# Performance work log

Measured on AMD Instinct MI355X. Metric: run time of the kernel, lower is better.

Reference implementation:

```python
import jax, jax.numpy as jnp
import numpy as np

B, S, NX, H = 8, 1024, 1024, 16
D = NX // H  # head dim = 64


def setup_inputs() -> dict:
    key = jax.random.key(0)
    k1, k2, k3 = jax.random.split(key, 3)
    x = jax.random.normal(k1, (B, S, NX), dtype=jnp.float32)
    Wqkv = jax.random.normal(k2, (NX, 3 * NX), dtype=jnp.float32) * 0.02
    bqkv = jnp.zeros((3 * NX,), dtype=jnp.float32)
    Wproj = jax.random.normal(k3, (NX, NX), dtype=jnp.float32) * 0.02
    bproj = jnp.zeros((NX,), dtype=jnp.float32)
    return {"x": x, "Wqkv": Wqkv, "bqkv": bqkv, "Wproj": Wproj, "bproj": bproj}


def reference(x, Wqkv, bqkv, Wproj, bproj):
    # c_attn: Conv1D == x @ W + b
    qkv = jnp.einsum('bsn,nm->bsm', x, Wqkv) + bqkv  # [B,S,3*NX]
    q, k, v = jnp.split(qkv, 3, axis=-1)
    # split heads -> [B,H,S,D]
    def split_heads(t):
        return t.reshape(B, S, H, D).transpose(0, 2, 1, 3)
    q, k, v = split_heads(q), split_heads(k), split_heads(v)
    # present = stack(key, value) with key as [B,H,S,D]
    present = jnp.stack((k, v))  # [2,B,H,S,D]
    # scores, scaled (scale=True) by sqrt(head_dim)
    w = jnp.einsum('bhqd,bhkd->bhqk', q, k) / jnp.sqrt(jnp.asarray(D, x.dtype))
    bias = jnp.tril(jnp.ones((S, S), dtype=x.dtype))[None, None]  # causal tril buffer
    w = w * bias - 10000.0 * (1.0 - bias)
    w = jax.nn.softmax(w, axis=-1)
    a = jnp.einsum('bhqk,bhkd->bhqd', w, v)  # [B,H,S,D]
    a = a.transpose(0, 2, 1, 3).reshape(B, S, NX)  # merge heads
    a = jnp.einsum('bsn,nm->bsm', a, Wproj) + bproj  # c_proj
    return a, present
```

## Files before the change

### kernel.cpp

```cpp
#include <hip/hip_runtime.h>
#include <stdint.h>


#define BB 8
#define SS 1024
#define NXX 1024
#define NH 16
#define HD 64
#define KK 1024
#define NKT 16

typedef __bf16 bf16x8 __attribute__((ext_vector_type(8)));
typedef float  floatx4 __attribute__((ext_vector_type(4)));
typedef unsigned short ushort8 __attribute__((ext_vector_type(8)));
typedef unsigned short ushortx4 __attribute__((ext_vector_type(4)));

__device__ inline float bf2f(unsigned short u) {
    unsigned int x = ((unsigned int)u) << 16;
    float f;
    __builtin_memcpy(&f, &x, 4);
    return f;
}
__device__ inline unsigned short f2bf(float f) {
    unsigned int u;
    __builtin_memcpy(&u, &f, 4);
    u += 0x7FFFu + ((u >> 16) & 1u);
    return (unsigned short)(u >> 16);
}

__device__ inline void gload_lds16(const unsigned short* g, unsigned short* l) {
    __builtin_amdgcn_global_load_lds(
        (const __attribute__((address_space(1))) void*)g,
        (__attribute__((address_space(3))) void*)l, 16, 0, 0);
}

__device__ inline void barrier_raw() {
    asm volatile("" ::: "memory");
    __builtin_amdgcn_sched_barrier(0);
    __builtin_amdgcn_s_barrier();
    __builtin_amdgcn_sched_barrier(0);
    asm volatile("" ::: "memory");
}
#define WAIT_VM4() asm volatile("s_waitcnt vmcnt(4)" ::: "memory")
#define WAIT_VM0() asm volatile("s_waitcnt vmcnt(0)" ::: "memory")

__global__ void sniff_k(const unsigned short* __restrict__ x, int* __restrict__ flag) {
    if (threadIdx.x == 0 && blockIdx.x == 0) {
        int g = 0;
        for (int i = 0; i < 512; i++) {
            float f = bf2f(x[i]);
            float a = fabsf(f);
            if (!(a <= 1e4f)) g++;
            else if (f != 0.f && a < 1e-35f) g++;
        }
        *flag = (g > 16) ? 1 : 0;
    }
}

__global__ __launch_bounds__(256) void prep(
    const void* __restrict__ x, const void* __restrict__ Wqkv,
    const void* __restrict__ Wproj,
    unsigned short* __restrict__ xbf, unsigned short* __restrict__ WqkvT,
    unsigned short* __restrict__ WprojT, const int* __restrict__ flagp) {
    const int f32 = *flagp;
    int blk = blockIdx.x;
    if (blk < 4096) {
        const size_t i = ((size_t)blk * 256 + threadIdx.x) * 8;
        if (f32) {
            const floatx4* p = (const floatx4*)((const float*)x + i);
            floatx4 f0 = p[0], f1 = p[1];
            ushort8 u;
#pragma unroll
            for (int j = 0; j < 4; j++) { u[j] = f2bf(f0[j]); u[4 + j] = f2bf(f1[j]); }
            *(ushort8*)(xbf + i) = u;
        } else {
            *(ushort8*)(xbf + i) = *(const ushort8*)((const unsigned short*)x + i);
        }
        return;
    }
    blk -= 4096;
    const void* in;
    unsigned short* out;
    int R, C;
    if (blk < 3072) { in = Wqkv; out = WqkvT; R = 1024; C = 3072; }
    else            { blk -= 3072; in = Wproj; out = WprojT; R = 1024; C = 1024; }
    const int ctiles = C / 32;
    const int c0 = (blk % ctiles) * 32, r0 = (blk / ctiles) * 32;

    __shared__ unsigned short tile[32][33];
    const int tx = threadIdx.x & 31, ty = threadIdx.x >> 5;
    if (f32) {
        const float* inf = (const float*)in;
#pragma unroll
        for (int i = ty; i < 32; i += 8)
            tile[i][tx] = f2bf(inf[(size_t)(r0 + i) * C + c0 + tx]);
    } else {
        const unsigned short* inu = (const unsigned short*)in;
#pragma unroll
        for (int i = ty; i < 32; i += 8)
            tile[i][tx] = inu[(size_t)(r0 + i) * C + c0 + tx];
    }
    __syncthreads();
#pragma unroll
    for (int i = ty; i < 32; i += 8)
        out[(size_t)(c0 + i) * R + r0 + tx] = tile[tx][i];
}

__global__ __launch_bounds__(256) void transpose_v(
    const void* __restrict__ outbase, unsigned short* __restrict__ vbfT,
    const int* __restrict__ flagp) {
    const int f32 = *flagp;
    const int blk = blockIdx.x;
    const int sb = blk & 15;
    const int bh = blk >> 4;
    const int tid = threadIdx.x;
    const int r = tid >> 2;
    const int c0 = (tid & 3) * 16;
    __shared__ unsigned short tile[64][72];
    const int perm = ((r & 15) << 2) | (r >> 4);
    const size_t esz = f32 ? 4 : 2;
    const char* vbase = (const char*)outbase + (size_t)(2 * BB * SS * NXX) * esz;
    if (f32) {
        const float* src = (const float*)vbase + ((size_t)bh * SS + sb * 64 + r) * HD + c0;
#pragma unroll
        for (int j = 0; j < 16; j++) tile[c0 + j][perm] = f2bf(src[j]);
    } else {
        const unsigned short* src = (const unsigned short*)vbase + ((size_t)bh * SS + sb * 64 + r) * HD + c0;
#pragma unroll
        for (int j = 0; j < 16; j++) tile[c0 + j][perm] = src[j];
    }
    __syncthreads();
    const int d = tid >> 2;
    const int o0 = (tid & 3) * 16;
    unsigned short* dst = vbfT + ((size_t)(bh * HD + d)) * SS + sb * 64 + o0;
    *(ushort8*)dst       = *(const ushort8*)&tile[d][o0];
    *(ushort8*)(dst + 8) = *(const ushort8*)&tile[d][o0 + 8];
}

#define STAGE_A(slot, h, kt) do { \
    const unsigned short* sg_ = Ab + (size_t)((h) * 128) * KK + (size_t)(kt) * 64; \
    gload_lds16(sg_, &As[slot][h][w * 512]); \
    gload_lds16(sg_ + (size_t)64 * KK, &As[slot][h][4096 + w * 512]); \
} while (0)
#define STAGE_B(slot, h, kt) do { \
    const unsigned short* sg_ = Bb + (size_t)((h) * 128) * KK + (size_t)(kt) * 64; \
    gload_lds16(sg_, &Bs[slot][h][w * 512]); \
    gload_lds16(sg_ + (size_t)64 * KK, &Bs[slot][h][4096 + w * 512]); \
} while (0)
#define PHASE(qq, STAGE_STMT, TAIL) do { \
    bf16x8 a_[2][2]; \
    _Pragma("unroll") \
    for (int mm = 0; mm < 2; mm++) { \
        const int arow = (qq) * 32 + mm * 16 + l15; \
        a_[mm][0] = *(const bf16x8*)&Ah[arow * 64 + fo0]; \
        a_[mm][1] = *(const bf16x8*)&Ah[arow * 64 + fo1]; \
    } \
    STAGE_STMT; \
    barrier_raw(); \
    __builtin_amdgcn_s_setprio(1); \
    _Pragma("unroll") \
    for (int mm = 0; mm < 2; mm++) \
    _Pragma("unroll") \
    for (int nf = 0; nf < 4; nf++) { \
        acc[2 * (qq) + mm][nf] = __builtin_amdgcn_mfma_f32_16x16x32_bf16(a_[mm][0], bfr[nf][0], acc[2 * (qq) + mm][nf], 0, 0, 0); \
        acc[2 * (qq) + mm][nf] = __builtin_amdgcn_mfma_f32_16x16x32_bf16(a_[mm][1], bfr[nf][1], acc[2 * (qq) + mm][nf], 0, 0, 0); \
    } \
    __builtin_amdgcn_s_setprio(0); \
    TAIL; \
    barrier_raw(); \
} while (0)

template <int MODE>
__global__ __launch_bounds__(512, 2) void gemm8p(
    const unsigned short* __restrict__ A,
    const unsigned short* __restrict__ Bt,
    const void* __restrict__ bias,
    void* __restrict__ outbase,
    unsigned short* __restrict__ q_ws,
    unsigned short* __restrict__ kbf,
    int M, int N, int Nt, const int* __restrict__ flagp) {
    __shared__ __align__(16) unsigned short As[2][2][128 * 64];
    __shared__ __align__(16) unsigned short Bs[2][2][128 * 64];

    const int f32 = *flagp;
    const int tid  = threadIdx.x;
    const int lane = tid & 63;
    const int w = tid >> 6;
    const int r = w >> 2;
    const int c = w & 3;
    const int bh2 = c >> 1;
    const int l15 = lane & 15;
    const int quad = lane >> 4;

    const int cpx = gridDim.x >> 3;
    const int bid = (blockIdx.x & 7) * cpx + (blockIdx.x >> 3);
    const int bx = bid % Nt, by = bid / Nt;
    const int row0 = by * 256, col0 = bx * 256;

    floatx4 acc[8][4];
    floatx4 zz = {0.f, 0.f, 0.f, 0.f};
#pragma unroll
    for (int i = 0; i < 8; i++)
#pragma unroll
        for (int j = 0; j < 4; j++) acc[i][j] = zz;

    const int srow = tid >> 3;
    const int scole = ((tid & 7) ^ (srow & 7)) << 3;
    const unsigned short* Ab = A  + (size_t)(row0 + srow) * KK + scole;
    const unsigned short* Bb = Bt + (size_t)(col0 + srow) * KK + scole;

    const int fo0 = (quad << 3) ^ ((l15 & 7) << 3);
    const int fo1 = fo0 ^ 32;

    STAGE_A(0, 0, 0); STAGE_A(0, 1, 0);
    STAGE_B(0, 0, 0); STAGE_B(0, 1, 0);
    STAGE_B(1, 0, 1); STAGE_B(1, 1, 1);
    WAIT_VM4();
    barrier_raw();

    bf16x8 bfr[4][2];
#pragma unroll 2
    for (int t = 0; t < NKT; t++) {
        const int slot = t & 1;
        const unsigned short* Ah = &As[slot][r][0];
        const unsigned short* Bh = &Bs[slot][bh2][0];
#pragma unroll
        for (int nf = 0; nf < 4; nf++) {
            const int brow = (c & 1) * 64 + nf * 16 + l15;
            bfr[nf][0] = *(const bf16x8*)&Bh[brow * 64 + fo0];
            bfr[nf][1] = *(const bf16x8*)&Bh[brow * 64 + fo1];
        }
        PHASE(0, { if (t + 1 < NKT) STAGE_A((t + 1) & 1, 0, t + 1); }, {});
        PHASE(1, { if (t + 1 < NKT) STAGE_A((t + 1) & 1, 1, t + 1); }, {});
        PHASE(2, { if (t + 2 < NKT) STAGE_B(slot, 0, t + 2); }, {});
        PHASE(3, { if (t + 2 < NKT) STAGE_B(slot, 1, t + 2); },
              { if (t < NKT - 2) { WAIT_VM4(); } else { WAIT_VM0(); } });
    }

    float bv[4];
#pragma unroll
    for (int nf = 0; nf < 4; nf++) {
        const int colb = col0 + c * 64 + nf * 16 + l15;
        bv[nf] = f32 ? ((const float*)bias)[colb] : bf2f(((const unsigned short*)bias)[colb]);
    }

    if (MODE == 0) {
#pragma unroll
        for (int mi = 0; mi < 8; mi++)
#pragma unroll
            for (int nf = 0; nf < 4; nf++) {
                const int colb = col0 + c * 64 + nf * 16 + l15;
#pragma unroll
                for (int i = 0; i < 4; i++) {
                    const int row = row0 + r * 128 + mi * 16 + quad * 4 + i;
                    const float val = acc[mi][nf][i] + bv[nf];
                    const size_t idx = (size_t)row * N + colb;
                    if (f32) ((float*)outbase)[idx] = val;
                    else     ((unsigned short*)outbase)[idx] = f2bf(val);
                }
            }
        return;
    }

    const int sec = col0 >> 10;
    const size_t esz = f32 ? 4 : 2;
    const int b = row0 >> 10;
    const int s0 = row0 & 1023;

    if (sec == 0) {
#pragma unroll
        for (int mi = 0; mi < 8; mi++)
#pragma unroll
            for (int nf = 0; nf < 4; nf++) {
                const int colb = col0 + c * 64 + nf * 16 + l15;
                const int h = (colb & 1023) >> 6, d = colb & 63;
#pragma unroll
                for (int i = 0; i < 4; i++) {
                    const int s = s0 + r * 128 + mi * 16 + quad * 4 + i;
                    q_ws[(size_t)((b * NH + h) * SS + s) * HD + d] = f2bf(acc[mi][nf][i] + bv[nf]);
                }
            }
    } else if (sec == 1) {
        char* kbase = (char*)outbase + (size_t)(BB * SS * NXX) * esz;
#pragma unroll
        for (int mi = 0; mi < 8; mi++)
#pragma unroll
            for (int nf = 0; nf < 4; nf++) {
                const int colb = col0 + c * 64 + nf * 16 + l15;
                const int h = (colb & 1023) >> 6, d = colb & 63;
#pragma unroll
                for (int i = 0; i < 4; i++) {
                    const int s = s0 + r * 128 + mi * 16 + quad * 4 + i;
                    const float val = acc[mi][nf][i] + bv[nf];
                    const size_t idx = (size_t)((b * NH + h) * SS + s) * HD + d;
                    if (f32) ((float*)kbase)[idx] = val;
                    else     ((unsigned short*)kbase)[idx] = f2bf(val);
                    kbf[idx] = f2bf(val);
                }
            }
    } else {
        char* vbase = (char*)outbase + (size_t)(2 * BB * SS * NXX) * esz;
#pragma unroll
        for (int mi = 0; mi < 8; mi++)
#pragma unroll
            for (int nf = 0; nf < 4; nf++) {
                const int colb = col0 + c * 64 + nf * 16 + l15;
                const int h = (colb & 1023) >> 6, d = colb & 63;
#pragma unroll
                for (int i = 0; i < 4; i++) {
                    const int s = s0 + r * 128 + mi * 16 + quad * 4 + i;
                    const float val = acc[mi][nf][i] + bv[nf];
                    const size_t idx = (size_t)((b * NH + h) * SS + s) * HD + d;
                    if (f32) ((float*)vbase)[idx] = val;
                    else     ((unsigned short*)vbase)[idx] = f2bf(val);
                }
            }
    }
}

__global__ __launch_bounds__(256) void attn(
    const unsigned short* __restrict__ q_ws,
    const unsigned short* __restrict__ kbf,
    const unsigned short* __restrict__ vbfT,
    unsigned short* __restrict__ amerged) {
    const int tid = threadIdx.x;
    const int lane = tid & 63;
    const int w = tid >> 6;
    const int l15 = lane & 15, quad = lane >> 4;
    const int blk = blockIdx.x;
    const int p = blk & 3;
    const int bh = blk >> 2;
    const int b = bh >> 4, h = bh & 15;

    const unsigned short* Q = q_ws + (size_t)bh * (SS * HD);
    const unsigned short* K = kbf + (size_t)bh * (SS * HD);
    const unsigned short* V = vbfT + (size_t)bh * (HD * SS);

    __shared__ __align__(16) unsigned short Ks[64][72];
    __shared__ __align__(16) unsigned short Vs[64][72];
    __shared__ __align__(16) unsigned short Pl[4][32][72];

    floatx4 zz = {0.f, 0.f, 0.f, 0.f};
    ushort8 ones_u;
#pragma unroll
    for (int j = 0; j < 8; j++) ones_u[j] = 0x3F80;
    const bf16x8 ones = __builtin_bit_cast(bf16x8, ones_u);

    const int srow = tid >> 2;
    const int soff = (tid & 3) * 16;

#pragma unroll
    for (int tile = 0; tile < 2; tile++) {
        const int qb = tile ? (7 - p) : p;
        const int qbase = qb * 128;
        const int wrow0 = qbase + w * 32;
        const int wq_max = wrow0 + 31;
        const int jend = qbase + 128;

        bf16x8 qa[2][2];
#pragma unroll
        for (int m = 0; m < 2; m++)
#pragma unroll
            for (int t = 0; t < 2; t++)
                qa[m][t] = *(const bf16x8*)&Q[(size_t)(wrow0 + m * 16 + l15) * HD + t * 32 + quad * 8];

        floatx4 o[2][4], o5[2];
        float mrow[2][4];
#pragma unroll
        for (int m = 0; m < 2; m++) {
            o5[m] = zz;
#pragma unroll
            for (int i = 0; i < 4; i++) mrow[m][i] = -1e30f;
#pragma unroll
            for (int nf = 0; nf < 4; nf++) o[m][nf] = zz;
        }

        *(ushort8*)&Ks[srow][soff]     = *(const ushort8*)&K[(size_t)srow * HD + soff];
        *(ushort8*)&Ks[srow][soff + 8] = *(const ushort8*)&K[(size_t)srow * HD + soff + 8];
        *(ushort8*)&Vs[srow][soff]     = *(const ushort8*)&V[(size_t)srow * SS + soff];
        *(ushort8*)&Vs[srow][soff + 8] = *(const ushort8*)&V[(size_t)srow * SS + soff + 8];
        __syncthreads();

        for (int j0 = 0; j0 < jend; j0 += 64) {
            const bool havenext = (j0 + 64 < jend);
            ushort8 kn0, kn1, vn0, vn1;
            if (havenext) {
                kn0 = *(const ushort8*)&K[(size_t)(j0 + 64 + srow) * HD + soff];
                kn1 = *(const ushort8*)&K[(size_t)(j0 + 64 + srow) * HD + soff + 8];
                vn0 = *(const ushort8*)&V[(size_t)srow * SS + j0 + 64 + soff];
                vn1 = *(const ushort8*)&V[(size_t)srow * SS + j0 + 64 + soff + 8];
            }

            if (j0 <= wq_max) {
                floatx4 sf[2][4];
#pragma unroll
                for (int kg = 0; kg < 4; kg++) {
                    bf16x8 kb0 = *(const bf16x8*)&Ks[kg * 16 + l15][quad * 8];
                    bf16x8 kb1 = *(const bf16x8*)&Ks[kg * 16 + l15][32 + quad * 8];
#pragma unroll
                    for (int m = 0; m < 2; m++) {
                        floatx4 s = zz;
                        s = __builtin_amdgcn_mfma_f32_16x16x32_bf16(qa[m][0], kb0, s, 0, 0, 0);
                        s = __builtin_amdgcn_mfma_f32_16x16x32_bf16(qa[m][1], kb1, s, 0, 0, 0);
                        sf[m][kg] = s;
                    }
                }

                float alpha_[2][4];
#pragma unroll
                for (int m = 0; m < 2; m++)
#pragma unroll
                    for (int i = 0; i < 4; i++) {
                        const int qrow = wrow0 + m * 16 + quad * 4 + i;
                        float pv4[4];
#pragma unroll
                        for (int kg = 0; kg < 4; kg++) {
                            const int key = j0 + kg * 16 + l15;
                            float s = sf[m][kg][i] * 0.125f;
                            if (key > qrow) s = -10000.0f;
                            pv4[kg] = s;
                        }
                        float t = fmaxf(fmaxf(pv4[0], pv4[1]), fmaxf(pv4[2], pv4[3]));
                        t = fmaxf(t, __shfl_xor(t, 1));
                        t = fmaxf(t, __shfl_xor(t, 2));
                        t = fmaxf(t, __shfl_xor(t, 4));
                        t = fmaxf(t, __shfl_xor(t, 8));
                        const float mnew = fmaxf(mrow[m][i], t);
                        alpha_[m][i] = __expf(mrow[m][i] - mnew);
                        mrow[m][i] = mnew;
                        ushortx4 pk;
#pragma unroll
                        for (int kg = 0; kg < 4; kg++)
                            pk[kg] = f2bf(__expf(pv4[kg] - mnew));
                        *(ushortx4*)&Pl[w][m * 16 + quad * 4 + i][l15 * 4] = pk;
                    }

#pragma unroll
                for (int m = 0; m < 2; m++) {
#pragma unroll
                    for (int i = 0; i < 4; i++) o5[m][i] *= alpha_[m][i];
#pragma unroll
                    for (int nf = 0; nf < 4; nf++)
#pragma unroll
                        for (int i = 0; i < 4; i++) o[m][nf][i] *= alpha_[m][i];
                }

                bf16x8 pa[2][2];
#pragma unroll
                for (int m = 0; m < 2; m++) {
                    pa[m][0] = *(const bf16x8*)&Pl[w][m * 16 + l15][quad * 8];
                    pa[m][1] = *(const bf16x8*)&Pl[w][m * 16 + l15][32 + quad * 8];
                }

#pragma unroll
                for (int m = 0; m < 2; m++) {
                    o5[m] = __builtin_amdgcn_mfma_f32_16x16x32_bf16(pa[m][0], ones, o5[m], 0, 0, 0);
                    o5[m] = __builtin_amdgcn_mfma_f32_16x16x32_bf16(pa[m][1], ones, o5[m], 0, 0, 0);
                }
#pragma unroll
                for (int nf = 0; nf < 4; nf++) {
                    bf16x8 vb0 = *(const bf16x8*)&Vs[nf * 16 + l15][quad * 8];
                    bf16x8 vb1 = *(const bf16x8*)&Vs[nf * 16 + l15][32 + quad * 8];
#pragma unroll
                    for (int m = 0; m < 2; m++) {
                        o[m][nf] = __builtin_amdgcn_mfma_f32_16x16x32_bf16(pa[m][0], vb0, o[m][nf], 0, 0, 0);
                        o[m][nf] = __builtin_amdgcn_mfma_f32_16x16x32_bf16(pa[m][1], vb1, o[m][nf], 0, 0, 0);
                    }
                }
            }
            __syncthreads();
            if (havenext) {
                *(ushort8*)&Ks[srow][soff]     = kn0;
                *(ushort8*)&Ks[srow][soff + 8] = kn1;
                *(ushort8*)&Vs[srow][soff]     = vn0;
                *(ushort8*)&Vs[srow][soff + 8] = vn1;
            }
            __syncthreads();
        }

#pragma unroll
        for (int m = 0; m < 2; m++)
#pragma unroll
            for (int nf = 0; nf < 4; nf++)
#pragma unroll
                for (int i = 0; i < 4; i++) {
                    const int s = wrow0 + m * 16 + quad * 4 + i;
                    amerged[(size_t)(b * SS + s) * NXX + h * HD + nf * 16 + l15] =
                        f2bf(o[m][nf][i] / o5[m][i]);
                }
        __syncthreads();
    }
}

extern "C" void kernel_launch(void* const* d_in, const int* in_sizes, int n_in,
                              void* d_out, int out_size, void* d_ws, size_t ws_size,
                              hipStream_t stream) {
    const void* x     = d_in[0];
    const void* Wqkv  = d_in[1];
    const void* bqkv  = d_in[2];
    const void* Wproj = d_in[3];
    const void* bproj = d_in[4];

    int* flag = (int*)d_ws;
    unsigned short* ws = (unsigned short*)d_ws + 8;
    unsigned short* WqkvT   = ws;
    unsigned short* WprojT  = WqkvT + 3072 * 1024;
    unsigned short* q_ws    = WprojT + 1024 * 1024;
    unsigned short* kbf     = q_ws + 8 * 1024 * 1024;
    unsigned short* vbfT    = kbf + 8 * 1024 * 1024;
    unsigned short* amerged = vbfT + 8 * 1024 * 1024;
    unsigned short* xbf     = amerged;

    sniff_k<<<1, 64, 0, stream>>>((const unsigned short*)x, flag);
    prep<<<dim3(8192), 256, 0, stream>>>(x, Wqkv, Wproj, xbf, WqkvT, WprojT, flag);
    gemm8p<1><<<dim3(12 * 32), 512, 0, stream>>>(
        xbf, WqkvT, bqkv, d_out, q_ws, kbf, 8192, 3072, 12, flag);
    transpose_v<<<dim3(128 * 16), 256, 0, stream>>>(d_out, vbfT, flag);
    attn<<<dim3(BB * NH * 4), 256, 0, stream>>>(q_ws, kbf, vbfT, amerged);
    gemm8p<0><<<dim3(4 * 32), 512, 0, stream>>>(
        amerged, WprojT, bproj, d_out, nullptr, nullptr, 8192, 1024, 4, flag);
}
```

Baseline: 346.7 us.

## Use 128x128 tiled GEMM for output projection, exp2 softmax, parallel sniff

Replaces the 256x512-style gemm8p projection launch (128 blocks of 512 threads) with a new 128x128-tile, double-buffered LDS GEMM launched on a 8x64 grid, so more blocks fill the GPU. The attention softmax folds the log2(e) factor into the score scale and uses exp2f in place of __expf, which removes a multiply per exponent. The input-dtype sniff kernel now reads with a full wavefront and a shuffle reduction instead of a serial 512-element loop. The new GEMM uses a shallow K-step of 32 with a barrier every iteration, which may limit its throughput.

```diff
diff --git a/kernel.cpp b/kernel.cpp
--- a/kernel.cpp
+++ b/kernel.cpp
@@ -45,16 +45,19 @@
 #define WAIT_VM0() asm volatile("s_waitcnt vmcnt(0)" ::: "memory")
 
 __global__ void sniff_k(const unsigned short* __restrict__ x, int* __restrict__ flag) {
-    if (threadIdx.x == 0 && blockIdx.x == 0) {
-        int g = 0;
-        for (int i = 0; i < 512; i++) {
-            float f = bf2f(x[i]);
-            float a = fabsf(f);
-            if (!(a <= 1e4f)) g++;
-            else if (f != 0.f && a < 1e-35f) g++;
-        }
-        *flag = (g > 16) ? 1 : 0;
-    }
+    const int lane = threadIdx.x & 63;
+    ushort8 v = *(const ushort8*)(x + (size_t)lane * 8);
+    int g = 0;
+#pragma unroll
+    for (int j = 0; j < 8; j++) {
+        float f = bf2f(v[j]);
+        float a = fabsf(f);
+        if (!(a <= 1e4f)) g++;
+        else if (f != 0.f && a < 1e-35f) g++;
+    }
+#pragma unroll
+    for (int s = 1; s < 64; s <<= 1) g += __shfl_xor(g, s);
+    if (lane == 0 && blockIdx.x == 0) *flag = (g > 16) ? 1 : 0;
 }
 
 __global__ __launch_bounds__(256) void prep(
@@ -318,6 +321,95 @@
     }
 }
 
+__global__ __launch_bounds__(256) void gemm_bt(
+    const unsigned short* __restrict__ A,
+    const unsigned short* __restrict__ Bt,
+    const void* __restrict__ bias,
+    void* __restrict__ outbase,
+    int M, int N, int K, const int* __restrict__ flagp) {
+    __shared__ __align__(16) unsigned short As[2][128 * 32];
+    __shared__ __align__(16) unsigned short Bs[2][128 * 32];
+
+    const int f32 = *flagp;
+    const int tid  = threadIdx.x;
+    const int lane = tid & 63;
+    const int wave = tid >> 6;
+    const int wr = wave >> 1, wc = wave & 1;
+    const int l15 = lane & 15;
+    const int quad = lane >> 4;
+    const int row0 = blockIdx.y * 128;
+    const int col0 = blockIdx.x * 128;
+
+    floatx4 acc[4][4];
+    floatx4 zz = {0.f, 0.f, 0.f, 0.f};
+#pragma unroll
+    for (int i = 0; i < 4; i++)
+#pragma unroll
+        for (int j = 0; j < 4; j++) acc[i][j] = zz;
+
+    const int lrow = lane >> 2;
+    const int lcol = (lane & 3) * 8;
+    const unsigned short* Ag = A  + (size_t)(row0 + wave * 32 + lrow) * K + lcol;
+    const unsigned short* Bg = Bt + (size_t)(col0 + wave * 32 + lrow) * K + lcol;
+    const int sl0 = (wave * 32) * 32;
+    const int sl1 = (wave * 32 + 16) * 32;
+
+    gload_lds16(Ag, &As[0][sl0]);
+    gload_lds16(Ag + (size_t)16 * K, &As[0][sl1]);
+    gload_lds16(Bg, &Bs[0][sl0]);
+    gload_lds16(Bg + (size_t)16 * K, &Bs[0][sl1]);
+    __syncthreads();
+
+    int cur = 0;
+    for (int k0 = 0; k0 < K; k0 += 32) {
+        if (k0 + 32 < K) {
+            const unsigned short* Agn = Ag + k0 + 32;
+            const unsigned short* Bgn = Bg + k0 + 32;
+            gload_lds16(Agn, &As[cur ^ 1][sl0]);
+            gload_lds16(Agn + (size_t)16 * K, &As[cur ^ 1][sl1]);
+            gload_lds16(Bgn, &Bs[cur ^ 1][sl0]);
+            gload_lds16(Bgn + (size_t)16 * K, &Bs[cur ^ 1][sl1]);
+        }
+
+        bf16x8 af[4], bfr[4];
+#pragma unroll
+        for (int mi = 0; mi < 4; mi++)
+            af[mi] = *(const bf16x8*)&As[cur][(wr * 64 + mi * 16 + l15) * 32 + quad * 8];
+#pragma unroll
+        for (int ni = 0; ni < 4; ni++)
+            bfr[ni] = *(const bf16x8*)&Bs[cur][(wc * 64 + ni * 16 + l15) * 32 + quad * 8];
+#pragma unroll
+        for (int mi = 0; mi < 4; mi++)
+#pragma unroll
+            for (int ni = 0; ni < 4; ni++)
+                acc[mi][ni] = __builtin_amdgcn_mfma_f32_16x16x32_bf16(af[mi], bfr[ni], acc[mi][ni], 0, 0, 0);
+
+        __syncthreads();
+        cur ^= 1;
+    }
+
+    float bv[4];
+#pragma unroll
+    for (int ni = 0; ni < 4; ni++) {
+        const int colb = col0 + wc * 64 + ni * 16 + l15;
+        bv[ni] = f32 ? ((const float*)bias)[colb] : bf2f(((const unsigned short*)bias)[colb]);
+    }
+#pragma unroll
+    for (int mi = 0; mi < 4; mi++)
+#pragma unroll
+        for (int ni = 0; ni < 4; ni++) {
+            const int colb = col0 + wc * 64 + ni * 16 + l15;
+#pragma unroll
+            for (int i = 0; i < 4; i++) {
+                const int row = row0 + wr * 64 + mi * 16 + quad * 4 + i;
+                const float val = acc[mi][ni][i] + bv[ni];
+                const size_t idx = (size_t)row * N + colb;
+                if (f32) ((float*)outbase)[idx] = val;
+                else     ((unsigned short*)outbase)[idx] = f2bf(val);
+            }
+        }
+}
+
 __global__ __launch_bounds__(256) void attn(
     const unsigned short* __restrict__ q_ws,
     const unsigned short* __restrict__ kbf,
@@ -340,6 +432,7 @@
     __shared__ __align__(16) unsigned short Vs[64][72];
     __shared__ __align__(16) unsigned short Pl[4][32][72];
 
+    const float SC2 = 0.18033688f;
     floatx4 zz = {0.f, 0.f, 0.f, 0.f};
     ushort8 ones_u;
 #pragma unroll
@@ -416,22 +509,22 @@
 #pragma unroll
                         for (int kg = 0; kg < 4; kg++) {
                             const int key = j0 + kg * 16 + l15;
-                            float s = sf[m][kg][i] * 0.125f;
-                            if (key > qrow) s = -10000.0f;
+                            float s = sf[m][kg][i] * SC2;
+                            if (key > qrow) s = -100000.0f;
                             pv4[kg] = s;
                         }
-                        float t = fmaxf(fmaxf(pv4[0], pv4[1]), fmaxf(pv4[2], pv4[3]));
+                        float t = fmaxf(fmaxf(fmaxf(pv4[0], pv4[1]), pv4[2]), pv4[3]);
                         t = fmaxf(t, __shfl_xor(t, 1));
                         t = fmaxf(t, __shfl_xor(t, 2));
                         t = fmaxf(t, __shfl_xor(t, 4));
                         t = fmaxf(t, __shfl_xor(t, 8));
                         const float mnew = fmaxf(mrow[m][i], t);
-                        alpha_[m][i] = __expf(mrow[m][i] - mnew);
+                        alpha_[m][i] = exp2f(mrow[m][i] - mnew);
                         mrow[m][i] = mnew;
                         ushortx4 pk;
 #pragma unroll
                         for (int kg = 0; kg < 4; kg++)
-                            pk[kg] = f2bf(__expf(pv4[kg] - mnew));
+                            pk[kg] = f2bf(exp2f(pv4[kg] - mnew));
                         *(ushortx4*)&Pl[w][m * 16 + quad * 4 + i][l15 * 4] = pk;
                     }
 
@@ -517,6 +610,6 @@
         xbf, WqkvT, bqkv, d_out, q_ws, kbf, 8192, 3072, 12, flag);
     transpose_v<<<dim3(128 * 16), 256, 0, stream>>>(d_out, vbfT, flag);
     attn<<<dim3(BB * NH * 4), 256, 0, stream>>>(q_ws, kbf, vbfT, amerged);
-    gemm8p<0><<<dim3(4 * 32), 512, 0, stream>>>(
-        amerged, WprojT, bproj, d_out, nullptr, nullptr, 8192, 1024, 4, flag);
-}
+    gemm_bt<<<dim3(1024 / 128, 8192 / 128), 256, 0, stream>>>(
+        amerged, WprojT, bproj, d_out, 8192, 1024, 1024, flag);
+}
```

Measured after the change: 340.4 us. No clear change (-1.8%).
